# Performance work log

Measured on AMD Instinct MI355X. Metric: run time of the kernel, lower is better.

Reference implementation:

```python
import jax, jax.numpy as jnp
import numpy as np

N_NODES = 100000
N_EDGES = 600000
D_IN = 128
D_OUT = 128


def setup_inputs() -> dict:
    key = jax.random.key(0)
    k1, k2, k3 = jax.random.split(key, 3)
    x = jax.random.normal(k1, (N_NODES, D_IN), dtype=jnp.float32)
    edge_index = jax.random.randint(k2, (2, N_EDGES), 0, N_NODES, dtype=jnp.int32)
    W = jax.random.normal(k3, (D_OUT, D_IN), dtype=jnp.float32) * 0.02
    b = jnp.zeros((D_OUT,), dtype=jnp.float32)
    return {"x": x, "edge_index": edge_index, "W": W, "b": b}


def reference(x, edge_index, W, b):
    # x: [N, D], edge_index: [2, E]
    n = x.shape[0]
    src = edge_index[0]
    dst = edge_index[1]
    # gather + elementwise abs diff: [E, D]
    msg = jnp.abs(x[src] - x[dst])
    # scatter-mean with out=x.clone(): sum includes the initial x values,
    # count is the number of scattered edges per node. Self-loops add a zero
    # message and +1 to the count, so counts = out_degree + 1 >= 1.
    sums = x + jax.ops.segment_sum(msg, src, num_segments=n)
    counts = jax.ops.segment_sum(jnp.ones_like(src, dtype=x.dtype), src, num_segments=n) + 1.0
    out = sums / counts[:, None]
    # Linear
    return out @ W.T + b
```

## Files before the change

kernel.cpp:

```cpp
#include <hip/hip_runtime.h>

#define D 128
#define CHB 8
#define CHSZ 256
#define TILE 2048
#define CAPCH 1856
#define SCAN_N 512
#define CAPQ 960
#define PADW 136
#define MAXDEG 32

#define QS   0.047244094f
#define QB   6.047244094f
#define IQS  21.16666667f

typedef __attribute__((ext_vector_type(8))) short bf16x8;
typedef __attribute__((ext_vector_type(4))) short bf16x4;
typedef __attribute__((ext_vector_type(4))) unsigned short u16x4;
typedef __attribute__((ext_vector_type(4))) float f32x4;

__device__ inline short f2bf(float f) {
    unsigned u = __float_as_uint(f);
    unsigned r = (u + 0x7fff + ((u >> 16) & 1)) >> 16;
    return (short)r;
}
__device__ inline bf16x8 pack8(float4 a, float4 b) {
    bf16x8 r;
    r[0] = f2bf(a.x); r[1] = f2bf(a.y); r[2] = f2bf(a.z); r[3] = f2bf(a.w);
    r[4] = f2bf(b.x); r[5] = f2bf(b.y); r[6] = f2bf(b.z); r[7] = f2bf(b.w);
    return r;
}
__device__ inline float bf2f(unsigned short h) {
    return __uint_as_float(((unsigned)h) << 16);
}
__device__ inline unsigned q8(float v) {
    int q = (int)rintf(v * IQS);
    q = q < -127 ? -127 : (q > 127 ? 127 : q);
    return (unsigned)(q + 128);
}

__global__ __launch_bounds__(256) void zero_ints(int* __restrict__ g, int n) {
    int i = blockIdx.x * 256 + threadIdx.x;
    if (i < n) g[i] = 0;
}

__global__ __launch_bounds__(256) void prep3(const float* __restrict__ x,
                                             unsigned short* __restrict__ xh,
                                             unsigned char* __restrict__ xq,
                                             const int* __restrict__ ei,
                                             int* __restrict__ gcur,
                                             int2* __restrict__ part,
                                             const float* __restrict__ Wg,
                                             bf16x8* __restrict__ Wpk,
                                             int N, int E, int NT, int NCH) {
    __shared__ int hist[SCAN_N];
    __shared__ int pref[SCAN_N];
    __shared__ int gbase[SCAN_N];
    __shared__ int2 sedge[TILE];
    int t = threadIdx.x;
    if ((int)blockIdx.x < NT) {
        int e0 = blockIdx.x * TILE;
        int cntT = E - e0; if (cntT > TILE) cntT = TILE;
        for (int i = t; i < SCAN_N; i += 256) hist[i] = 0;
        __syncthreads();

        int src[8], dst[8], rk[8];
        int base8 = e0 + t * 8;
        if (base8 + 8 <= E) {
            int4 s0 = *(const int4*)(ei + base8);
            int4 s1 = *(const int4*)(ei + base8 + 4);
            int4 d0 = *(const int4*)(ei + E + base8);
            int4 d1 = *(const int4*)(ei + E + base8 + 4);
            src[0]=s0.x; src[1]=s0.y; src[2]=s0.z; src[3]=s0.w;
            src[4]=s1.x; src[5]=s1.y; src[6]=s1.z; src[7]=s1.w;
            dst[0]=d0.x; dst[1]=d0.y; dst[2]=d0.z; dst[3]=d0.w;
            dst[4]=d1.x; dst[5]=d1.y; dst[6]=d1.z; dst[7]=d1.w;
        } else {
#pragma unroll
            for (int k = 0; k < 8; ++k) {
                int g = base8 + k;
                src[k] = (g < E) ? ei[g] : 0;
                dst[k] = (g < E) ? ei[E + g] : 0;
            }
        }
#pragma unroll
        for (int k = 0; k < 8; ++k) {
            rk[k] = (t * 8 + k < cntT) ? atomicAdd(&hist[src[k] >> CHB], 1) : -1;
        }
        __syncthreads();
        if (t == 0) {
            int acc = 0;
            for (int i = 0; i < SCAN_N; ++i) { pref[i] = acc; acc += hist[i]; }
        }
        __syncthreads();
        for (int c = t; c < NCH; c += 256)
            gbase[c] = hist[c] ? atomicAdd(&gcur[c], hist[c]) : 0;
#pragma unroll
        for (int k = 0; k < 8; ++k)
            if (rk[k] >= 0)
                sedge[pref[src[k] >> CHB] + rk[k]] = make_int2(src[k], dst[k]);
        __syncthreads();
        for (int i = t; i < cntT; i += 256) {
            int2 e = sedge[i];
            int c = e.x >> CHB;
            int slot = gbase[c] + (i - pref[c]);
            if (slot < CAPCH) part[(size_t)c * CAPCH + slot] = e;
        }
    } else if ((int)blockIdx.x == NT) {
        for (int i = t; i < 2048; i += 256) {
            int f = i >> 6, l = i & 63;
            int n16 = f >> 2, kk = f & 3;
            int c = n16 * 16 + (l & 15);
            int k0 = kk * 32 + (l >> 4) * 8;
            float4 p0 = *(const float4*)(Wg + c * D + k0);
            float4 p1 = *(const float4*)(Wg + c * D + k0 + 4);
            Wpk[i] = pack8(p0, p1);
        }
    } else {
        long idx = (long)(blockIdx.x - NT - 1) * 256 + t;
        long total = (long)N * D / 8;
        if (idx < total) {
            const float4* xp = (const float4*)x;
            float4 p0 = xp[idx * 2];
            float4 p1 = xp[idx * 2 + 1];
            ((bf16x8*)xh)[idx] = pack8(p0, p1);
            unsigned lo = q8(p0.x) | (q8(p0.y) << 8) | (q8(p0.z) << 16) | (q8(p0.w) << 24);
            unsigned hi = q8(p1.x) | (q8(p1.y) << 8) | (q8(p1.z) << 16) | (q8(p1.w) << 24);
            ((uint2*)xq)[idx] = make_uint2(lo, hi);
        }
    }
}

__global__ __launch_bounds__(256) void aggmm(const unsigned short* __restrict__ xh,
                                             const unsigned char* __restrict__ xq,
                                             const int* __restrict__ gcur,
                                             const int2* __restrict__ part,
                                             const bf16x8* __restrict__ Wpk,
                                             const float* __restrict__ bvec,
                                             float* __restrict__ out, int N) {
    __shared__ int nh[64];
    __shared__ int off[65];
    __shared__ int adj[CAPQ];
    __shared__ __align__(16) short tile[64 * PADW];
    int t = threadIdx.x;
    int ch = blockIdx.x >> 2;
    int sub = blockIdx.x & 3;
    int nbase = (ch << CHB) + sub * 64;
    int cnt = gcur[ch]; if (cnt > CAPCH) cnt = CAPCH;
    if (t < 64) nh[t] = 0;
    __syncthreads();

    int2 e2[8]; int rk2[8];
#pragma unroll
    for (int ii = 0; ii < 8; ++ii) {
        int i = ii * 256 + t;
        rk2[ii] = -1;
        if (i < cnt) {
            int2 e = part[(size_t)ch * CAPCH + i];
            int rl = e.x & (CHSZ - 1);
            if ((rl >> 6) == sub) {
                e2[ii] = e;
                rk2[ii] = atomicAdd(&nh[rl & 63], 1);
            }
        }
    }
    __syncthreads();
    if (t == 0) {
        int acc = 0;
        for (int i = 0; i < 64; ++i) { off[i] = acc; acc += nh[i]; }
        off[64] = acc;
    }
    __syncthreads();
#pragma unroll
    for (int ii = 0; ii < 8; ++ii)
        if (rk2[ii] >= 0) {
            int idx = off[e2[ii].x & 63] + rk2[ii];
            if (idx < CAPQ) adj[idx] = e2[ii].y;
        }
    __syncthreads();

    int team = t >> 5, lane = t & 31;
    for (int rl = team; rl < 64; rl += 8) {
        int r = nbase + rl;
        bf16x4* lp = (bf16x4*)&tile[rl * PADW + lane * 4];
        if (r >= N) { bf16x4 z = {0, 0, 0, 0}; *lp = z; continue; }
        int deg = nh[rl];
        int ab = off[rl];
        int dg = deg;
        if (ab + dg > CAPQ) dg = CAPQ - ab;
        if (dg < 0) dg = 0;
        u16x4 ah = *(const u16x4*)(xh + (size_t)r * D + lane * 4);
        float ax = bf2f(ah[0]), ay = bf2f(ah[1]);
        float az = bf2f(ah[2]), aw = bf2f(ah[3]);
        float px = ax + QB, py = ay + QB, pz = az + QB, pw = aw + QB;
        float4 c0 = {0,0,0,0}, c1 = {0,0,0,0}, c2 = {0,0,0,0}, c3 = {0,0,0,0};
        for (int f = 0; f < dg; f += 4) {
            int d0 = adj[ab + f];
            int d1 = (f + 1 < dg) ? adj[ab + f + 1] : d0;
            int d2 = (f + 2 < dg) ? adj[ab + f + 2] : d0;
            int d3 = (f + 3 < dg) ? adj[ab + f + 3] : d0;
            float m1 = (f + 1 < dg) ? 1.0f : 0.0f;
            float m2 = (f + 2 < dg) ? 1.0f : 0.0f;
            float m3 = (f + 3 < dg) ? 1.0f : 0.0f;
            unsigned q0 = *(const unsigned*)(xq + (size_t)d0 * D + lane * 4);
            unsigned q1 = *(const unsigned*)(xq + (size_t)d1 * D + lane * 4);
            unsigned q2 = *(const unsigned*)(xq + (size_t)d2 * D + lane * 4);
            unsigned q3 = *(const unsigned*)(xq + (size_t)d3 * D + lane * 4);
#define ACCQ(cc, qq, mm)                                                     \
            cc.x = fmaf(fabsf(fmaf((float)( qq        & 0xFFu), -QS, px)), mm, cc.x); \
            cc.y = fmaf(fabsf(fmaf((float)((qq >>  8) & 0xFFu), -QS, py)), mm, cc.y); \
            cc.z = fmaf(fabsf(fmaf((float)((qq >> 16) & 0xFFu), -QS, pz)), mm, cc.z); \
            cc.w = fmaf(fabsf(fmaf((float)((qq >> 24) & 0xFFu), -QS, pw)), mm, cc.w);
            ACCQ(c0, q0, 1.0f)
            ACCQ(c1, q1, m1)
            ACCQ(c2, q2, m2)
            ACCQ(c3, q3, m3)
#undef ACCQ
        }
        float s = 1.0f / (float)(deg + 1);
        bf16x4 p;
        p[0] = f2bf((ax + ((c0.x + c1.x) + (c2.x + c3.x))) * s);
        p[1] = f2bf((ay + ((c0.y + c1.y) + (c2.y + c3.y))) * s);
        p[2] = f2bf((az + ((c0.z + c1.z) + (c2.z + c3.z))) * s);
        p[3] = f2bf((aw + ((c0.w + c1.w) + (c2.w + c3.w))) * s);
        *lp = p;
    }

    __syncthreads();

    int w = t >> 6;
    int l = t & 63;
    int rw = w >> 1, cw = w & 1;
    int l15 = l & 15, lk8 = (l >> 4) * 8;

    bf16x8 Af[2][4];
#pragma unroll
    for (int m = 0; m < 2; ++m) {
        int row = rw * 32 + m * 16 + l15;
#pragma unroll
        for (int kk = 0; kk < 4; ++kk)
            Af[m][kk] = *(const bf16x8*)&tile[row * PADW + kk * 32 + lk8];
    }

    f32x4 acc[2][4] = {};
#pragma unroll
    for (int n = 0; n < 4; ++n) {
        int col16 = cw * 4 + n;
#pragma unroll
        for (int kk = 0; kk < 4; ++kk) {
            bf16x8 Bf = Wpk[(col16 * 4 + kk) * 64 + l];
            acc[0][n] = __builtin_amdgcn_mfma_f32_16x16x32_bf16(Af[0][kk], Bf, acc[0][n], 0, 0, 0);
            acc[1][n] = __builtin_amdgcn_mfma_f32_16x16x32_bf16(Af[1][kk], Bf, acc[1][n], 0, 0, 0);
        }
    }

#pragma unroll
    for (int m = 0; m < 2; ++m) {
        int r0 = nbase + rw * 32 + m * 16 + (l >> 4) * 4;
#pragma unroll
        for (int n = 0; n < 4; ++n) {
            int c = cw * 64 + n * 16 + l15;
            float bias = bvec[c];
#pragma unroll
            for (int j = 0; j < 4; ++j) {
                int r = r0 + j;
                if (r < N) out[(size_t)r * D + c] = acc[m][n][j] + bias;
            }
        }
    }
}

__global__ __launch_bounds__(256) void bucket_fb(const int* __restrict__ ei,
                                                 int* __restrict__ cnt,
                                                 int* __restrict__ bucket, int E) {
    int e = blockIdx.x * 256 + threadIdx.x;
    if (e >= E) return;
    int src = ei[e];
    int dst = ei[E + e];
    int pos = atomicAdd(&cnt[src], 1);
    if (pos < MAXDEG) bucket[src * MAXDEG + pos] = dst;
}

__global__ __launch_bounds__(256) void agg_f32(const float* __restrict__ x,
                                               const int* __restrict__ cnt,
                                               const int* __restrict__ bucket,
                                               float* __restrict__ y, int N) {
    int t = blockIdx.x * 256 + threadIdx.x;
    int team = t >> 5;
    int lane = t & 31;
    if (team >= N) return;
    int r = team;
    int deg = cnt[r];
    float4 a = ((const float4*)(x + (size_t)r * D))[lane];
    int m = deg < MAXDEG ? deg : MAXDEG;
    const int* bk = bucket + (size_t)r * MAXDEG;
    float4 a0 = a, a1 = {0,0,0,0}, a2 = {0,0,0,0}, a3 = {0,0,0,0};
    for (int j = 0; j < m; j += 4) {
        int4 d4 = *(const int4*)(bk + j);
        int d0 = d4.x;
        int d1 = (j + 1 < m) ? d4.y : r;
        int d2 = (j + 2 < m) ? d4.z : r;
        int d3 = (j + 3 < m) ? d4.w : r;
        float4 v0 = ((const float4*)(x + (size_t)d0 * D))[lane];
        float4 v1 = ((const float4*)(x + (size_t)d1 * D))[lane];
        float4 v2 = ((const float4*)(x + (size_t)d2 * D))[lane];
        float4 v3 = ((const float4*)(x + (size_t)d3 * D))[lane];
        a0.x += fabsf(a.x - v0.x); a0.y += fabsf(a.y - v0.y);
        a0.z += fabsf(a.z - v0.z); a0.w += fabsf(a.w - v0.w);
        a1.x += fabsf(a.x - v1.x); a1.y += fabsf(a.y - v1.y);
        a1.z += fabsf(a.z - v1.z); a1.w += fabsf(a.w - v1.w);
        a2.x += fabsf(a.x - v2.x); a2.y += fabsf(a.y - v2.y);
        a2.z += fabsf(a.z - v2.z); a2.w += fabsf(a.w - v2.w);
        a3.x += fabsf(a.x - v3.x); a3.y += fabsf(a.y - v3.y);
        a3.z += fabsf(a.z - v3.z); a3.w += fabsf(a.w - v3.w);
    }
    float s = 1.0f / (float)(deg + 1);
    float4 o;
    o.x = ((a0.x + a1.x) + (a2.x + a3.x)) * s;
    o.y = ((a0.y + a1.y) + (a2.y + a3.y)) * s;
    o.z = ((a0.z + a1.z) + (a2.z + a3.z)) * s;
    o.w = ((a0.w + a1.w) + (a2.w + a3.w)) * s;
    ((float4*)(y + (size_t)r * D))[lane] = o;
}

__global__ __launch_bounds__(256) void mfma_f32(const float* y,
                                                const float* __restrict__ W,
                                                const float* __restrict__ b,
                                                float* out, int N) {
    int w = threadIdx.x >> 6;
    int l = threadIdx.x & 63;
    int rw = w >> 1;
    int cw = w & 1;
    int l15 = l & 15;
    int lk8 = (l >> 4) * 8;
    bf16x8 Bf[4][4];
    float bias[4];
#pragma unroll
    for (int n = 0; n < 4; ++n) {
        int c = cw * 64 + n * 16 + l15;
        const float* wr = W + c * D;
        bias[n] = b[c];
#pragma unroll
        for (int kk = 0; kk < 4; ++kk) {
            float4 p0 = *(const float4*)(wr + kk * 32 + lk8);
            float4 p1 = *(const float4*)(wr + kk * 32 + lk8 + 4);
            Bf[n][kk] = pack8(p0, p1);
        }
    }
    int rowbase = blockIdx.x * 64 + rw * 32;
    bf16x8 Af[2][4];
#pragma unroll
    for (int m = 0; m < 2; ++m) {
        int r = rowbase + m * 16 + l15;
        int rc = r < N ? r : N - 1;
        const float* yr = y + (size_t)rc * D;
#pragma unroll
        for (int kk = 0; kk < 4; ++kk) {
            float4 p0 = *(const float4*)(yr + kk * 32 + lk8);
            float4 p1 = *(const float4*)(yr + kk * 32 + lk8 + 4);
            Af[m][kk] = pack8(p0, p1);
        }
    }
    f32x4 acc[2][4] = {};
#pragma unroll
    for (int m = 0; m < 2; ++m)
#pragma unroll
        for (int n = 0; n < 4; ++n)
#pragma unroll
            for (int kk = 0; kk < 4; ++kk)
                acc[m][n] = __builtin_amdgcn_mfma_f32_16x16x32_bf16(
                    Af[m][kk], Bf[n][kk], acc[m][n], 0, 0, 0);
#pragma unroll
    for (int m = 0; m < 2; ++m) {
        int r0 = rowbase + m * 16 + (l >> 4) * 4;
#pragma unroll
        for (int n = 0; n < 4; ++n) {
            int c = cw * 64 + n * 16 + l15;
#pragma unroll
            for (int j = 0; j < 4; ++j) {
                int r = r0 + j;
                if (r < N) out[(size_t)r * D + c] = acc[m][n][j] + bias[n];
            }
        }
    }
}

extern "C" void kernel_launch(void* const* d_in, const int* in_sizes, int n_in,
                              void* d_out, int out_size, void* d_ws, size_t ws_size,
                              hipStream_t stream) {
    const float* x  = (const float*)d_in[0];
    const int*   ei = (const int*)d_in[1];
    const float* W  = (const float*)d_in[2];
    const float* b  = (const float*)d_in[3];
    float* out = (float*)d_out;

    int N = in_sizes[0] / D;
    int E = in_sizes[1] / 2;

    int NCH = (N + CHSZ - 1) >> CHB;
    int NT  = (E + TILE - 1) / TILE;

    char* ws = (char*)d_ws;
    unsigned short* xh = (unsigned short*)ws;
    unsigned char* xq = (unsigned char*)(ws + (size_t)N * D * 2);
    int2* part = (int2*)(ws + (size_t)N * D * 3);
    int* gcur = (int*)(part + (size_t)NCH * CAPCH);
    size_t wpo = (((size_t)((char*)(gcur + NCH) - ws)) + 255) & ~(size_t)255;
    bf16x8* Wpk = (bf16x8*)(ws + wpo);
    size_t need = wpo + 32768;

    bool ok = (ws_size >= need) && (NCH <= SCAN_N);

    if (ok) {
        zero_ints<<<(NCH + 255) / 256, 256, 0, stream>>>(gcur, NCH);
        long conv_threads = (long)N * D / 8;
        int cblocks = (int)((conv_threads + 255) / 256);
        prep3<<<NT + 1 + cblocks, 256, 0, stream>>>(x, xh, xq, ei, gcur, part, W,
                                                    Wpk, N, E, NT, NCH);
        aggmm<<<NCH * 4, 256, 0, stream>>>(xh, xq, gcur, part, Wpk, b, out, N);
    } else {
        int* cnt    = (int*)d_ws;
        int* bucket = cnt + N;
        int teams_per_block = 256 / 32;
        int ablocks = (N + teams_per_block - 1) / teams_per_block;
        zero_ints<<<(N + 255) / 256, 256, 0, stream>>>(cnt, N);
        bucket_fb<<<(E + 255) / 256, 256, 0, stream>>>(ei, cnt, bucket, E);
        agg_f32<<<ablocks, 256, 0, stream>>>(x, cnt, bucket, out, N);
        mfma_f32<<<(N + 63) / 64, 256, 0, stream>>>(out, W, b, out, N);
    }
}
```

Before: 81.50 us.

## Split neighbor gather across wave quarter-groups and stage source rows in LDS

```diff
diff --git a/kernel.cpp b/kernel.cpp
--- a/kernel.cpp
+++ b/kernel.cpp
@@ -8,6 +8,7 @@
 #define SCAN_N 512
 #define CAPQ 960
 #define PADW 136
+#define SRCW 136
 #define MAXDEG 32
 
 #define QS   0.047244094f
@@ -141,7 +142,9 @@
     __shared__ int nh[64];
     __shared__ int off[65];
     __shared__ int adj[CAPQ];
-    __shared__ __align__(16) short tile[64 * PADW];
+    __shared__ __align__(16) unsigned short srcS[64 * SRCW];
+    __shared__ __align__(16) short tileh[64 * PADW];
+
     int t = threadIdx.x;
     int ch = blockIdx.x >> 2;
     int sub = blockIdx.x & 3;
@@ -170,6 +173,13 @@
         for (int i = 0; i < 64; ++i) { off[i] = acc; acc += nh[i]; }
         off[64] = acc;
     }
+    for (int i = t; i < 2048; i += 256) {
+        int row = i >> 5, q = i & 31;
+        int r = nbase + row;
+        int rc = r < N ? r : N - 1;
+        u16x4 v = *(const u16x4*)(xh + (size_t)rc * D + q * 4);
+        *(u16x4*)(srcS + row * SRCW + q * 4) = v;
+    }
     __syncthreads();
 #pragma unroll
     for (int ii = 0; ii < 8; ++ii)
@@ -179,57 +189,73 @@
         }
     __syncthreads();
 
-    int team = t >> 5, lane = t & 31;
-    for (int rl = team; rl < 64; rl += 8) {
+    int wv = t >> 6;
+    int l  = t & 63;
+    int g  = l >> 4;
+    int c16 = l & 15;
+    for (int rl = wv; rl < 64; rl += 4) {
         int r = nbase + rl;
-        bf16x4* lp = (bf16x4*)&tile[rl * PADW + lane * 4];
-        if (r >= N) { bf16x4 z = {0, 0, 0, 0}; *lp = z; continue; }
+        if (r >= N) {
+            if (l < 16) {
+                bf16x4 z = {0, 0, 0, 0};
+                *(bf16x4*)&tileh[rl * PADW + c16 * 8] = z;
+                *(bf16x4*)&tileh[rl * PADW + c16 * 8 + 4] = z;
+            }
+            continue;
+        }
         int deg = nh[rl];
         int ab = off[rl];
         int dg = deg;
         if (ab + dg > CAPQ) dg = CAPQ - ab;
         if (dg < 0) dg = 0;
-        u16x4 ah = *(const u16x4*)(xh + (size_t)r * D + lane * 4);
-        float ax = bf2f(ah[0]), ay = bf2f(ah[1]);
-        float az = bf2f(ah[2]), aw = bf2f(ah[3]);
-        float px = ax + QB, py = ay + QB, pz = az + QB, pw = aw + QB;
-        float4 c0 = {0,0,0,0}, c1 = {0,0,0,0}, c2 = {0,0,0,0}, c3 = {0,0,0,0};
+
+        u16x4 sv0 = *(const u16x4*)(srcS + rl * SRCW + c16 * 8);
+        u16x4 sv1 = *(const u16x4*)(srcS + rl * SRCW + c16 * 8 + 4);
+        float s0 = bf2f(sv0[0]), s1 = bf2f(sv0[1]);
+        float s2 = bf2f(sv0[2]), s3 = bf2f(sv0[3]);
+        float s4 = bf2f(sv1[0]), s5 = bf2f(sv1[1]);
+        float s6 = bf2f(sv1[2]), s7 = bf2f(sv1[3]);
+        float p0 = s0 + QB, p1 = s1 + QB, p2 = s2 + QB, p3 = s3 + QB;
+        float p4 = s4 + QB, p5 = s5 + QB, p6 = s6 + QB, p7 = s7 + QB;
+        float c0 = 0, c1 = 0, c2 = 0, c3 = 0, c4 = 0, c5 = 0, c6 = 0, c7 = 0;
+
         for (int f = 0; f < dg; f += 4) {
-            int d0 = adj[ab + f];
-            int d1 = (f + 1 < dg) ? adj[ab + f + 1] : d0;
-            int d2 = (f + 2 < dg) ? adj[ab + f + 2] : d0;
-            int d3 = (f + 3 < dg) ? adj[ab + f + 3] : d0;
-            float m1 = (f + 1 < dg) ? 1.0f : 0.0f;
-            float m2 = (f + 2 < dg) ? 1.0f : 0.0f;
-            float m3 = (f + 3 < dg) ? 1.0f : 0.0f;
-            unsigned q0 = *(const unsigned*)(xq + (size_t)d0 * D + lane * 4);
-            unsigned q1 = *(const unsigned*)(xq + (size_t)d1 * D + lane * 4);
-            unsigned q2 = *(const unsigned*)(xq + (size_t)d2 * D + lane * 4);
-            unsigned q3 = *(const unsigned*)(xq + (size_t)d3 * D + lane * 4);
-#define ACCQ(cc, qq, mm)                                                     \
-            cc.x = fmaf(fabsf(fmaf((float)( qq        & 0xFFu), -QS, px)), mm, cc.x); \
-            cc.y = fmaf(fabsf(fmaf((float)((qq >>  8) & 0xFFu), -QS, py)), mm, cc.y); \
-            cc.z = fmaf(fabsf(fmaf((float)((qq >> 16) & 0xFFu), -QS, pz)), mm, cc.z); \
-            cc.w = fmaf(fabsf(fmaf((float)((qq >> 24) & 0xFFu), -QS, pw)), mm, cc.w);
-            ACCQ(c0, q0, 1.0f)
-            ACCQ(c1, q1, m1)
-            ACCQ(c2, q2, m2)
-            ACCQ(c3, q3, m3)
-#undef ACCQ
-        }
-        float s = 1.0f / (float)(deg + 1);
-        bf16x4 p;
-        p[0] = f2bf((ax + ((c0.x + c1.x) + (c2.x + c3.x))) * s);
-        p[1] = f2bf((ay + ((c0.y + c1.y) + (c2.y + c3.y))) * s);
-        p[2] = f2bf((az + ((c0.z + c1.z) + (c2.z + c3.z))) * s);
-        p[3] = f2bf((aw + ((c0.w + c1.w) + (c2.w + c3.w))) * s);
-        *lp = p;
-    }
-
+            int idx = f + g;
+            float m = (idx < dg) ? 1.0f : 0.0f;
+            int d = (idx < dg) ? adj[ab + idx] : adj[ab + f];
+            uint2 qv = *(const uint2*)(xq + (size_t)d * D + c16 * 8);
+            c0 = fmaf(fabsf(fmaf((float)( qv.x        & 0xFFu), -QS, p0)), m, c0);
+            c1 = fmaf(fabsf(fmaf((float)((qv.x >>  8) & 0xFFu), -QS, p1)), m, c1);
+            c2 = fmaf(fabsf(fmaf((float)((qv.x >> 16) & 0xFFu), -QS, p2)), m, c2);
+            c3 = fmaf(fabsf(fmaf((float)((qv.x >> 24) & 0xFFu), -QS, p3)), m, c3);
+            c4 = fmaf(fabsf(fmaf((float)( qv.y        & 0xFFu), -QS, p4)), m, c4);
+            c5 = fmaf(fabsf(fmaf((float)((qv.y >>  8) & 0xFFu), -QS, p5)), m, c5);
+            c6 = fmaf(fabsf(fmaf((float)((qv.y >> 16) & 0xFFu), -QS, p6)), m, c6);
+            c7 = fmaf(fabsf(fmaf((float)((qv.y >> 24) & 0xFFu), -QS, p7)), m, c7);
+        }
+        c0 += __shfl_xor(c0, 16); c0 += __shfl_xor(c0, 32);
+        c1 += __shfl_xor(c1, 16); c1 += __shfl_xor(c1, 32);
+        c2 += __shfl_xor(c2, 16); c2 += __shfl_xor(c2, 32);
+        c3 += __shfl_xor(c3, 16); c3 += __shfl_xor(c3, 32);
+        c4 += __shfl_xor(c4, 16); c4 += __shfl_xor(c4, 32);
+        c5 += __shfl_xor(c5, 16); c5 += __shfl_xor(c5, 32);
+        c6 += __shfl_xor(c6, 16); c6 += __shfl_xor(c6, 32);
+        c7 += __shfl_xor(c7, 16); c7 += __shfl_xor(c7, 32);
+
+        float inv = 1.0f / (float)(deg + 1);
+        if (l < 16) {
+            bf16x4 o0, o1;
+            o0[0] = f2bf((s0 + c0) * inv); o0[1] = f2bf((s1 + c1) * inv);
+            o0[2] = f2bf((s2 + c2) * inv); o0[3] = f2bf((s3 + c3) * inv);
+            o1[0] = f2bf((s4 + c4) * inv); o1[1] = f2bf((s5 + c5) * inv);
+            o1[2] = f2bf((s6 + c6) * inv); o1[3] = f2bf((s7 + c7) * inv);
+            *(bf16x4*)&tileh[rl * PADW + c16 * 8] = o0;
+            *(bf16x4*)&tileh[rl * PADW + c16 * 8 + 4] = o1;
+        }
+    }
     __syncthreads();
 
     int w = t >> 6;
-    int l = t & 63;
     int rw = w >> 1, cw = w & 1;
     int l15 = l & 15, lk8 = (l >> 4) * 8;
 
@@ -239,7 +265,7 @@
         int row = rw * 32 + m * 16 + l15;
 #pragma unroll
         for (int kk = 0; kk < 4; ++kk)
-            Af[m][kk] = *(const bf16x8*)&tile[row * PADW + kk * 32 + lk8];
+            Af[m][kk] = *(const bf16x8*)&tileh[row * PADW + kk * 32 + lk8];
     }
 
     f32x4 acc[2][4] = {};
```

Measured after the change: 101.1 us. 1.24x slower.
